# Performance work log

Hardware: AMD Instinct MI355X
Metric: run time of the kernel (lower is better)

Reference implementation:

```python
import jax, jax.numpy as jnp
import numpy as np
from jax import lax

SR = 7
HEADS = 8
EPS = 1e-5

def dwconv(x, w):
    # x: [B,C,H,W], w: [C,1,3,3] depthwise
    return lax.conv_general_dilated(x, w, (1, 1), 'SAME',
                                    feature_group_count=x.shape[1],
                                    dimension_numbers=('NCHW', 'OIHW', 'NCHW'))

def bn(x, g, b, m, v):
    # eval-mode BatchNorm2d over channel dim of [B,C,H,W]
    scale = g / jnp.sqrt(v + EPS)
    return x * scale[:, None, None] + (b - m * scale)[:, None, None]

def avgpool(x, k):
    B, C, H, W = x.shape
    return x.reshape(B, C, H // k, k, W // k, k).mean(axis=(3, 5))

def upsample(x, k):
    B, C, H, W = x.shape
    return jax.image.resize(x, (B, C, H * k, W * k), method='bilinear')


def setup_inputs() -> dict:
    key = jax.random.key(0)
    ks = jax.random.split(key, 12)
    B, N, C = 16, 3136, 256
    d = {}
    d['x'] = jax.random.normal(ks[0], (B, N, C), jnp.float32)
    d['Wv'] = jax.random.normal(ks[1], (C, C), jnp.float32) * 0.05
    d['conv1_w'] = jax.random.normal(ks[2], (C, 1, 3, 3), jnp.float32) * 0.05
    d['bn1_g'] = jnp.ones((C,), jnp.float32)
    d['bn1_b'] = jnp.zeros((C,), jnp.float32)
    d['bn1_m'] = jax.random.normal(ks[3], (C,), jnp.float32) * 0.05
    d['bn1_v'] = jax.random.uniform(ks[4], (C,), jnp.float32, 0.5, 1.5)
    d['conv2_w'] = jax.random.normal(ks[5], (C, 1, 3, 3), jnp.float32) * 0.05
    d['bn2_g'] = jnp.ones((C,), jnp.float32)
    d['bn2_b'] = jnp.zeros((C,), jnp.float32)
    d['bn2_m'] = jax.random.normal(ks[6], (C,), jnp.float32) * 0.05
    d['bn2_v'] = jax.random.uniform(ks[7], (C,), jnp.float32, 0.5, 1.5)
    d['vup_w'] = jax.random.normal(ks[8], (C, 1, 3, 3), jnp.float32) * 0.05
    d['bn3_g'] = jnp.ones((C,), jnp.float32)
    d['bn3_b'] = jnp.zeros((C,), jnp.float32)
    d['bn3_m'] = jax.random.normal(ks[9], (C,), jnp.float32) * 0.05
    d['bn3_v'] = jax.random.uniform(ks[10], (C,), jnp.float32, 0.5, 1.5)
    d['Wp'] = jax.random.normal(ks[11], (C, C), jnp.float32) * 0.05
    d['bp'] = jnp.zeros((C,), jnp.float32)
    return d


def reference(x, Wv, conv1_w, bn1_g, bn1_b, bn1_m, bn1_v,
              conv2_w, bn2_g, bn2_b, bn2_m, bn2_v,
              vup_w, bn3_g, bn3_b, bn3_m, bn3_v, Wp, bp):
    B, N, C = x.shape
    h = w = int(np.sqrt(N))
    hd = C // HEADS
    scale = C ** (-0.5)

    v = x @ Wv.T                                    # [B,N,C] (torch Linear, no bias)
    skip = v.reshape(B, h, w, C).transpose(0, 3, 1, 2)  # [B,C,h,w]

    s1 = bn(dwconv(skip, conv1_w), bn1_g, bn1_b, bn1_m, bn1_v)
    q = avgpool(s1, SR)                             # [B,C,h_,w_]
    s2 = bn(dwconv(jax.nn.gelu(s1, approximate=False), conv2_w),
            bn2_g, bn2_b, bn2_m, bn2_v)
    k = avgpool(s2, SR)                             # [B,C,h_,w_]
    skip_tok = jax.nn.gelu(s2, approximate=False).reshape(B, C, N).transpose(0, 2, 1)

    h_, w_ = h // SR, w // SR
    N_ = h_ * w_
    qh = q.reshape(B, HEADS, hd, N_).transpose(0, 1, 3, 2)   # [B,H,N_,d]
    kh = k.reshape(B, HEADS, hd, N_).transpose(0, 1, 3, 2)   # [B,H,N_,d]
    vh = v.reshape(B, N, HEADS, hd).transpose(0, 2, 1, 3)    # [B,H,N,d]

    attn = jnp.einsum('bhnd,bhmd->bhnm', qh, kh)             # [B,H,N_,N_]
    attn = attn.reshape(B * HEADS, N_, h_, w_)
    attn = upsample(attn, SR) * scale                        # [B*H,N_,h,w]
    attn = attn.reshape(B, HEADS, N_, N)
    attn = jax.nn.softmax(attn, axis=-1)

    o = jnp.einsum('bhnm,bhmd->bhnd', attn, vh)              # [B,H,N_,d]
    o = o.reshape(B, HEADS, h_, w_, hd).transpose(0, 1, 4, 2, 3).reshape(B, C, h_, w_)
    o = bn(dwconv(upsample(o, SR), vup_w), bn3_g, bn3_b, bn3_m, bn3_v)  # [B,C,h,w]

    out = o.reshape(B, C, N).transpose(0, 2, 1) + skip_tok
    out = out @ Wp.T + bp
    return out
```

## Files before the change

kernel.cpp:

```cpp
#include <hip/hip_runtime.h>
#include <math.h>

#define B_     16
#define H_IMG  56
#define W_IMG  56
#define N_TOK  3136
#define C_     256
#define C4_    64
#define NHEAD  8
#define HDIM   32
#define NCH    8

typedef float f32x4 __attribute__((ext_vector_type(4)));
typedef __bf16 bf16x8 __attribute__((ext_vector_type(8)));

__device__ __forceinline__ float geluf(float x) {
    return 0.5f * x * (1.0f + erff(x * 0.70710678118654752f));
}

__device__ __forceinline__ void up_coef(int o, int& i0, int& i1, float& t) {
    float f  = (float)(o - 3) * (1.0f / 7.0f);
    float fl = floorf(f);
    int   ii = (int)fl;
    t = f - fl;
    if (ii < 0)       { i0 = 0; i1 = 0; t = 0.0f; }
    else if (ii >= 7) { i0 = 7; i1 = 7; t = 0.0f; }
    else              { i0 = ii; i1 = ii + 1; }
}

__device__ __forceinline__ void split_bf16(float4 f, uint2& hi, uint2& lo) {
    unsigned u0 = __float_as_uint(f.x), u1 = __float_as_uint(f.y);
    unsigned u2 = __float_as_uint(f.z), u3 = __float_as_uint(f.w);
    unsigned h0 = u0 & 0xFFFF0000u, h1 = u1 & 0xFFFF0000u;
    unsigned h2 = u2 & 0xFFFF0000u, h3 = u3 & 0xFFFF0000u;
    hi = make_uint2((h0 >> 16) | h1, (h2 >> 16) | h3);
    float l0 = f.x - __uint_as_float(h0);
    float l1 = f.y - __uint_as_float(h1);
    float l2 = f.z - __uint_as_float(h2);
    float l3 = f.w - __uint_as_float(h3);
    lo = make_uint2((__float_as_uint(l0) >> 16) | (__float_as_uint(l1) & 0xFFFF0000u),
                    (__float_as_uint(l2) >> 16) | (__float_as_uint(l3) & 0xFFFF0000u));
}

__device__ __forceinline__ unsigned pack2_bf16(float a, float b) {
    __bf16 ha = (__bf16)a, hb = (__bf16)b;
    unsigned short ua = __builtin_bit_cast(unsigned short, ha);
    unsigned short ub = __builtin_bit_cast(unsigned short, hb);
    return (unsigned)ua | ((unsigned)ub << 16);
}

__device__ __forceinline__ void gload_lds16(const float* g, float* l) {
    __builtin_amdgcn_global_load_lds(
        (const __attribute__((address_space(1))) unsigned int*)g,
        (__attribute__((address_space(3))) unsigned int*)l, 16, 0, 0);
}

__global__ void prep_kernel(
    const float* __restrict__ w1, const float* __restrict__ w2, const float* __restrict__ w3,
    const float* __restrict__ g1, const float* __restrict__ b1, const float* __restrict__ m1, const float* __restrict__ v1,
    const float* __restrict__ g2, const float* __restrict__ b2, const float* __restrict__ m2, const float* __restrict__ v2,
    const float* __restrict__ g3, const float* __restrict__ b3, const float* __restrict__ m3, const float* __restrict__ v3,
    float* __restrict__ wT1, float* __restrict__ wT2, float* __restrict__ wT3,
    float* __restrict__ sc1, float* __restrict__ sh1,
    float* __restrict__ sc2, float* __restrict__ sh2,
    float* __restrict__ sc3, float* __restrict__ sh3)
{
    int c = threadIdx.x;
#pragma unroll
    for (int t = 0; t < 9; ++t) {
        wT1[t * C_ + c] = w1[c * 9 + t];
        wT2[t * C_ + c] = w2[c * 9 + t];
        wT3[t * C_ + c] = w3[c * 9 + t];
    }
    float s1 = g1[c] * rsqrtf(v1[c] + 1e-5f); sc1[c] = s1; sh1[c] = b1[c] - m1[c] * s1;
    float s2 = g2[c] * rsqrtf(v2[c] + 1e-5f); sc2[c] = s2; sh2[c] = b2[c] - m2[c] * s2;
    float s3 = g3[c] * rsqrtf(v3[c] + 1e-5f); sc3[c] = s3; sh3[c] = b3[c] - m3[c] * s3;
}

__global__ __launch_bounds__(256, 2) void gemm_nt_mfma_kernel(
    const float* __restrict__ A,
    const float* __restrict__ Bm,
    const float* __restrict__ bias,
    float* __restrict__ C,
    int M, int N)
{
    __shared__ float lds[8192];
    const int tid  = threadIdx.x;
    const int nb   = N >> 7;
    const int bx   = blockIdx.x % nb;
    const int by   = blockIdx.x / nb;
    const int lane = tid & 63;
    const int wv   = tid >> 6;
    const int wr   = wv >> 1, wc = wv & 1;
    const int l15  = lane & 15, kb = lane >> 4;

    const float* Abase = A  + (size_t)(by * 128) * 256;
    const float* Bbase = Bm + (size_t)(bx * 128) * 256;

    f32x4 acc[4][4];
#pragma unroll
    for (int m = 0; m < 4; ++m)
#pragma unroll
        for (int n = 0; n < 4; ++n) acc[m][n] = (f32x4)(0.0f);

    int srow[4], ssk[4];
#pragma unroll
    for (int i = 0; i < 4; ++i) {
        int u = i * 256 + tid;
        srow[i] = u >> 3;
        ssk[i]  = ((u & 7) ^ (srow[i] & 7)) << 2;
    }

#pragma unroll
    for (int k0 = 0; k0 < 256; k0 += 32) {
        __syncthreads();
#pragma unroll
        for (int i = 0; i < 4; ++i) {
            int u = i * 256 + tid;
            gload_lds16(Abase + (size_t)srow[i] * 256 + k0 + ssk[i], &lds[u * 4]);
        }
#pragma unroll
        for (int i = 0; i < 4; ++i) {
            int u = i * 256 + tid;
            gload_lds16(Bbase + (size_t)srow[i] * 256 + k0 + ssk[i], &lds[4096 + u * 4]);
        }
        __syncthreads();

        bf16x8 ah[4], al[4], bh[4], bl[4];
#pragma unroll
        for (int m = 0; m < 4; ++m) {
            int r = wr * 64 + m * 16 + l15;
            float4 f0 = *(const float4*)&lds[r * 32 + ((((kb * 2)    ) ^ (r & 7)) << 2)];
            float4 f1 = *(const float4*)&lds[r * 32 + ((((kb * 2) + 1) ^ (r & 7)) << 2)];
            uint2 h0, l0, h1, l1;
            split_bf16(f0, h0, l0);
            split_bf16(f1, h1, l1);
            ah[m] = __builtin_bit_cast(bf16x8, make_uint4(h0.x, h0.y, h1.x, h1.y));
            al[m] = __builtin_bit_cast(bf16x8, make_uint4(l0.x, l0.y, l1.x, l1.y));
        }
#pragma unroll
        for (int n = 0; n < 4; ++n) {
            int r = wc * 64 + n * 16 + l15;
            float4 f0 = *(const float4*)&lds[4096 + r * 32 + ((((kb * 2)    ) ^ (r & 7)) << 2)];
            float4 f1 = *(const float4*)&lds[4096 + r * 32 + ((((kb * 2) + 1) ^ (r & 7)) << 2)];
            uint2 h0, l0, h1, l1;
            split_bf16(f0, h0, l0);
            split_bf16(f1, h1, l1);
            bh[n] = __builtin_bit_cast(bf16x8, make_uint4(h0.x, h0.y, h1.x, h1.y));
            bl[n] = __builtin_bit_cast(bf16x8, make_uint4(l0.x, l0.y, l1.x, l1.y));
        }
#pragma unroll
        for (int m = 0; m < 4; ++m)
#pragma unroll
            for (int n = 0; n < 4; ++n) {
                acc[m][n] = __builtin_amdgcn_mfma_f32_16x16x32_bf16(ah[m], bh[n], acc[m][n], 0, 0, 0);
                acc[m][n] = __builtin_amdgcn_mfma_f32_16x16x32_bf16(ah[m], bl[n], acc[m][n], 0, 0, 0);
                acc[m][n] = __builtin_amdgcn_mfma_f32_16x16x32_bf16(al[m], bh[n], acc[m][n], 0, 0, 0);
            }
    }

    const int rb = by * 128 + wr * 64 + kb * 4;
    const int cb = bx * 128 + wc * 64 + l15;
#pragma unroll
    for (int n = 0; n < 4; ++n) {
        int col = cb + n * 16;
        float bv = bias ? bias[col] : 0.0f;
#pragma unroll
        for (int m = 0; m < 4; ++m) {
            int row = rb + m * 16;
#pragma unroll
            for (int r = 0; r < 4; ++r)
                C[(size_t)(row + r) * N + col] = acc[m][n][r] + bv;
        }
    }
}

__global__ __launch_bounds__(256, 4) void dwconv_bn_pool_gelu_kernel(
    const float* __restrict__ in, const float* __restrict__ wT,
    const float* __restrict__ scv, const float* __restrict__ shv,
    float* __restrict__ outg, float* __restrict__ pool)
{
    const int blk = blockIdx.x;
    const int xcd = blk & 7;
    const int j   = blk >> 3;
    const int b   = xcd + 8 * (j >> 6);
    const int g   = j & 63;
    const int gy  = g >> 3, gx = g & 7;
    const int tid = threadIdx.x;
    const int c4  = tid & 63;
    const int wv  = tid >> 6;
    const int c0  = c4 * 4;

    float4 wr[9];
#pragma unroll
    for (int t = 0; t < 9; ++t) wr[t] = *(const float4*)(wT + t * C_ + c0);
    const float4 sc = *(const float4*)(scv + c0);
    const float4 sh = *(const float4*)(shv + c0);

    const int x0 = gx * 7, y0 = gy * 7;
    const float* inb = in + (size_t)b * N_TOK * C_;
    float4 acc = make_float4(0, 0, 0, 0);

    for (int p = wv; p < 49; p += 4) {
        int py = p / 7, px = p - py * 7;
        int y = y0 + py, x = x0 + px;
        float cx = 0.f, cy = 0.f, cz = 0.f, cw = 0.f;
#pragma unroll
        for (int dy = -1; dy <= 1; ++dy) {
            int yy = y + dy;
            if (yy < 0 || yy >= H_IMG) continue;
#pragma unroll
            for (int dx = -1; dx <= 1; ++dx) {
                int xx = x + dx;
                if (xx < 0 || xx >= W_IMG) continue;
                const float4 iv = *(const float4*)(inb + (size_t)(yy * W_IMG + xx) * C_ + c0);
                const float4 w  = wr[(dy + 1) * 3 + (dx + 1)];
                cx = fmaf(iv.x, w.x, cx);
                cy = fmaf(iv.y, w.y, cy);
                cz = fmaf(iv.z, w.z, cz);
                cw = fmaf(iv.w, w.w, cw);
            }
        }
        float vx = cx * sc.x + sh.x;
        float vy = cy * sc.y + sh.y;
        float vz = cz * sc.z + sh.z;
        float vw = cw * sc.w + sh.w;
        acc.x += vx; acc.y += vy; acc.z += vz; acc.w += vw;
        *(float4*)(outg + ((size_t)b * N_TOK + y * W_IMG + x) * C_ + c0) =
            make_float4(geluf(vx), geluf(vy), geluf(vz), geluf(vw));
    }

    __shared__ float4 ps[4][64];
    ps[wv][c4] = acc;
    __syncthreads();
    if (tid < 64) {
        float4 s  = ps[0][tid];
        float4 t1 = ps[1][tid];
        float4 t2 = ps[2][tid];
        float4 t3 = ps[3][tid];
        const float r = 1.0f / 49.0f;
        *(float4*)(pool + ((size_t)b * 64 + g) * C_ + tid * 4) = make_float4(
            (s.x + t1.x + t2.x + t3.x) * r, (s.y + t1.y + t2.y + t3.y) * r,
            (s.z + t1.z + t2.z + t3.z) * r, (s.w + t1.w + t2.w + t3.w) * r);
    }
}

__global__ __launch_bounds__(256, 3) void dwconv_up_bn_add_kernel(
    const float* __restrict__ osm,
    const float* __restrict__ wT,
    const float* __restrict__ scv, const float* __restrict__ shv,
    const float* __restrict__ add_,
    float* __restrict__ out)
{
    const int blk = blockIdx.x;
    const int xcd = blk & 7;
    const int j   = blk >> 3;
    const int b   = xcd + 8 * (j >> 6);
    const int g   = j & 63;
    const int gy  = g >> 3, gx = g & 7;
    const int tid = threadIdx.x;
    const int c4  = tid & 63;
    const int wv  = tid >> 6;
    const int c0  = c4 * 4;

    float4 wr[9];
#pragma unroll
    for (int t = 0; t < 9; ++t) wr[t] = *(const float4*)(wT + t * C_ + c0);
    const float4 sc = *(const float4*)(scv + c0);
    const float4 sh = *(const float4*)(shv + c0);

    const float* ob = osm + (size_t)b * 64 * C_ + c0;
    const int cry0 = max(gy - 1, 0), cry1 = gy, cry2 = min(gy + 1, 7);
    const int crx0 = max(gx - 1, 0), crx1 = gx, crx2 = min(gx + 1, 7);

    for (int cpass = 0; cpass < 2; ++cpass) {
        const int xi = wv + cpass * 4;
        if (xi >= 7) break;
        const int x = gx * 7 + xi;

        float xt[3]; int rixv[3]; bool xval[3];
#pragma unroll
        for (int e = 0; e < 3; ++e) {
            int xx = x - 1 + e;
            xval[e] = (xx >= 0 && xx < W_IMG);
            if (xval[e]) {
                int i0, i1; float t;
                up_coef(xx, i0, i1, t);
                rixv[e] = i0 - gx + 1;
                xt[e]   = t;
            } else { rixv[e] = 0; xt[e] = 0.f; }
        }

        float4 CX[3][3];
#pragma unroll
        for (int ri = 0; ri < 3; ++ri) {
            const int rowc = (ri == 0) ? cry0 : ((ri == 1) ? cry1 : cry2);
            const float4 p0 = *(const float4*)(ob + (size_t)(rowc * 8 + crx0) * C_);
            const float4 p1 = *(const float4*)(ob + (size_t)(rowc * 8 + crx1) * C_);
            const float4 p2 = *(const float4*)(ob + (size_t)(rowc * 8 + crx2) * C_);
#pragma unroll
            for (int e = 0; e < 3; ++e) {
                const bool h2 = rixv[e] != 0;
                float lox = h2 ? p1.x : p0.x, hix = h2 ? p2.x : p1.x;
                float loy = h2 ? p1.y : p0.y, hiy = h2 ? p2.y : p1.y;
                float loz = h2 ? p1.z : p0.z, hiz = h2 ? p2.z : p1.z;
                float low = h2 ? p1.w : p0.w, hiw = h2 ? p2.w : p1.w;
                const float t = xt[e];
                float vx = fmaf(t, hix - lox, lox);
                float vy = fmaf(t, hiy - loy, loy);
                float vz = fmaf(t, hiz - loz, loz);
                float vw = fmaf(t, hiw - low, low);
                if (!xval[e]) { vx = vy = vz = vw = 0.f; }
                CX[ri][e] = make_float4(vx, vy, vz, vw);
            }
        }

#define UPROW(YY, U)                                                          \
        {                                                                     \
            int i0_, i1_; float t_;                                           \
            up_coef((YY), i0_, i1_, t_);                                      \
            const bool h2_ = (i0_ - gy + 1) != 0;                             \
            _Pragma("unroll")                                                 \
            for (int e = 0; e < 3; ++e) {                                     \
                const float4 lo = h2_ ? CX[1][e] : CX[0][e];                  \
                const float4 hi = h2_ ? CX[2][e] : CX[1][e];                  \
                U[e] = make_float4(fmaf(t_, hi.x - lo.x, lo.x),               \
                                   fmaf(t_, hi.y - lo.y, lo.y),               \
                                   fmaf(t_, hi.z - lo.z, lo.z),               \
                                   fmaf(t_, hi.w - lo.w, lo.w));              \
            }                                                                 \
        }

        float4 Um[3], U0[3], Up[3];
        UPROW(gy * 7 - 1, Um);
        UPROW(gy * 7,     U0);
#pragma unroll
        for (int y7 = 0; y7 < 7; ++y7) {
            const int y = gy * 7 + y7;
            UPROW(y + 1, Up);
            float ax = 0.f, ay = 0.f, az = 0.f, aw = 0.f;
            if (!(gy == 0 && y7 == 0)) {
#pragma unroll
                for (int e = 0; e < 3; ++e) {
                    const float4 w = wr[e];
                    ax = fmaf(Um[e].x, w.x, ax); ay = fmaf(Um[e].y, w.y, ay);
                    az = fmaf(Um[e].z, w.z, az); aw = fmaf(Um[e].w, w.w, aw);
                }
            }
#pragma unroll
            for (int e = 0; e < 3; ++e) {
                const float4 w = wr[3 + e];
                ax = fmaf(U0[e].x, w.x, ax); ay = fmaf(U0[e].y, w.y, ay);
                az = fmaf(U0[e].z, w.z, az); aw = fmaf(U0[e].w, w.w, aw);
            }
            if (!(gy == 7 && y7 == 6)) {
#pragma unroll
                for (int e = 0; e < 3; ++e) {
                    const float4 w = wr[6 + e];
                    ax = fmaf(Up[e].x, w.x, ax); ay = fmaf(Up[e].y, w.y, ay);
                    az = fmaf(Up[e].z, w.z, az); aw = fmaf(Up[e].w, w.w, aw);
                }
            }
            const size_t pix = (size_t)b * N_TOK + (size_t)y * W_IMG + x;
            const float4 av = *(const float4*)(add_ + pix * C_ + c0);
            *(float4*)(out + pix * C_ + c0) = make_float4(
                ax * sc.x + sh.x + av.x, ay * sc.y + sh.y + av.y,
                az * sc.z + sh.z + av.z, aw * sc.w + sh.w + av.w);
#pragma unroll
            for (int e = 0; e < 3; ++e) { Um[e] = U0[e]; U0[e] = Up[e]; }
        }
#undef UPROW
    }
}

__global__ __launch_bounds__(256) void qk_kernel(
    const float* __restrict__ q, const float* __restrict__ k,
    float* __restrict__ attnL, float* __restrict__ mrow_g)
{
    int bh = blockIdx.x;
    int b = bh >> 3, head = bh & 7;
    __shared__ float qs[64][33];
    __shared__ float ks[64][33];
    int tid = threadIdx.x;
    for (int t = tid; t < 512; t += 256) {
        int i = t >> 3, dq = (t & 7) * 4;
        const float4 qv = *(const float4*)(q + ((size_t)(b * 64 + i) * C_ + head * 32 + dq));
        const float4 kv = *(const float4*)(k + ((size_t)(b * 64 + i) * C_ + head * 32 + dq));
        qs[i][dq + 0] = qv.x; qs[i][dq + 1] = qv.y; qs[i][dq + 2] = qv.z; qs[i][dq + 3] = qv.w;
        ks[i][dq + 0] = kv.x; ks[i][dq + 1] = kv.y; ks[i][dq + 2] = kv.z; ks[i][dq + 3] = kv.w;
    }
    __syncthreads();
    int i  = tid >> 2;
    int jb = (tid & 3) * 16;
    float qr[32];
#pragma unroll
    for (int d = 0; d < 32; ++d) qr[d] = qs[i][d];
    float* outp = attnL + (size_t)bh * 4096 + i * 64 + jb;
    float mloc = -1e30f;
#pragma unroll
    for (int j = 0; j < 16; ++j) {
        float s = 0.f;
#pragma unroll
        for (int d = 0; d < 32; ++d) s = fmaf(qr[d], ks[jb + j][d], s);
        float sv = s * 0.0625f;
        outp[j] = sv;
        mloc = fmaxf(mloc, sv);
    }
    mloc = fmaxf(mloc, __shfl_xor(mloc, 1));
    mloc = fmaxf(mloc, __shfl_xor(mloc, 2));
    if ((tid & 3) == 0) mrow_g[bh * 64 + i] = mloc;
}

#define S_ALS 0
#define S_P   1792
#define S_VH  4096
#define S_VL  5248
#define S_RY  6400
#define S_ZP  7168
__global__ __launch_bounds__(256, 4) void attn_pv_kernel(
    const float* __restrict__ attnL,
    const float* __restrict__ mrow_g,
    const float* __restrict__ v,
    float* __restrict__ part_o,
    float* __restrict__ part_z)
{
    __shared__ unsigned sm[7424];
    float* smf = (float*)sm;

    const int blk   = blockIdx.x;
    const int xcd   = blk & 7;
    const int r8    = blk >> 3;
    const int b     = xcd + 8 * (r8 >> 6);
    const int rem   = r8 & 63;
    const int head  = rem >> 3;
    const int chunk = rem & 7;
    const int bh    = b * 8 + head;
    const int jb    = min(max(chunk - 1, 0), 5);

    const int tid  = threadIdx.x;
    const int lane = tid & 63;
    const int w    = tid >> 6;
    const int l15  = lane & 15, kb = lane >> 4;
    const int i    = tid >> 2;
    const int dg   = tid & 3;

    for (int u = tid; u < 384; u += 256) {
        int row = u / 6, cc = u % 6;
        float4 va = *(const float4*)(attnL + (size_t)bh * 4096 + row * 64 + jb * 8 + cc * 4);
        *(float4*)&smf[S_ALS + row * 28 + cc * 4] = va;
    }
    sm[S_P + (tid >> 2) * 36 + 28 + (tid & 3)] = 0;
    {
        int base = (tid < 128) ? S_VH : S_VL;
        int q2 = tid & 127;
        sm[base + (q2 >> 2) * 36 + 28 + (q2 & 3)] = 0;
    }
    const float mr = mrow_g[bh * 64 + i];

    int   x0a[14]; float txa[14];
#pragma unroll
    for (int j = 0; j < 14; ++j) {
        int i0, i1; float t;
        up_coef(dg * 14 + j, i0, i1, t);
        x0a[j] = i0; txa[j] = t;
    }

    f32x4 acc[2];
    acc[0] = (f32x4)(0.0f); acc[1] = (f32x4)(0.0f);
    float zacc = 0.0f;

    for (int rr = 0; rr < 7; ++rr) {
        const int y = chunk * 7 + rr;
        __syncthreads();

        float4 va, vb;
        if (tid < 224) {
            int x2 = tid >> 3, d0 = (tid & 7) * 4;
            const float* vp = v + ((size_t)b * N_TOK + y * W_IMG + 2 * x2) * C_ + head * 32 + d0;
            va = *(const float4*)vp;
            vb = *(const float4*)(vp + C_);
        }
        {
            int y0, y1; float ty;
            up_coef(y, y0, y1, ty);
#pragma unroll
            for (int kk2 = dg; kk2 < 9; kk2 += 4) {
                int ks2 = kk2 < 8 ? kk2 : 7;
                float a0 = smf[S_ALS + i * 28 + (y0 - jb) * 8 + ks2];
                float a1 = smf[S_ALS + i * 28 + (y1 - jb) * 8 + ks2];
                smf[S_RY + i * 12 + kk2] = fmaf(ty, a1 - a0, a0) - mr;
            }
        }
        if (tid < 224) {
            int x2 = tid >> 3, d0 = (tid & 7) * 4;
            float ae[4] = {va.x, va.y, va.z, va.w};
            float be[4] = {vb.x, vb.y, vb.z, vb.w};
#pragma unroll
            for (int j = 0; j < 4; ++j) {
                unsigned ua = __float_as_uint(ae[j]), ha = ua & 0xFFFF0000u;
                unsigned ub = __float_as_uint(be[j]), hb2 = ub & 0xFFFF0000u;
                sm[S_VH + (d0 + j) * 36 + x2] = (ha >> 16) | hb2;
                float la = ae[j] - __uint_as_float(ha);
                float lb = be[j] - __uint_as_float(hb2);
                sm[S_VL + (d0 + j) * 36 + x2] =
                    (__float_as_uint(la) >> 16) | (__float_as_uint(lb) & 0xFFFF0000u);
            }
        }
        __syncthreads();

#pragma unroll
        for (int j = 0; j < 7; ++j) {
            float r0 = smf[S_RY + i * 12 + x0a[2 * j]];
            float r1 = smf[S_RY + i * 12 + x0a[2 * j] + 1];
            float l0 = fmaf(txa[2 * j], r1 - r0, r0);
            float r2 = smf[S_RY + i * 12 + x0a[2 * j + 1]];
            float r3 = smf[S_RY + i * 12 + x0a[2 * j + 1] + 1];
            float l1 = fmaf(txa[2 * j + 1], r3 - r2, r2);
            float p0 = __expf(l0), p1 = __expf(l1);
            zacc += p0 + p1;
            sm[S_P + i * 36 + dg * 7 + j] = pack2_bf16(p0, p1);
        }
        __syncthreads();

#pragma unroll
        for (int s = 0; s < 2; ++s) {
            bf16x8 pa = *(const bf16x8*)&sm[S_P + (w * 16 + l15) * 36 + s * 16 + kb * 4];
#pragma unroll
            for (int n = 0; n < 2; ++n) {
                bf16x8 bhv = *(const bf16x8*)&sm[S_VH + (n * 16 + l15) * 36 + s * 16 + kb * 4];
                bf16x8 blv = *(const bf16x8*)&sm[S_VL + (n * 16 + l15) * 36 + s * 16 + kb * 4];
                acc[n] = __builtin_amdgcn_mfma_f32_16x16x32_bf16(pa, bhv, acc[n], 0, 0, 0);
                acc[n] = __builtin_amdgcn_mfma_f32_16x16x32_bf16(pa, blv, acc[n], 0, 0, 0);
            }
        }
    }

    smf[S_ZP + i * 4 + dg] = zacc;
    __syncthreads();
    if (tid < 64) {
        float zt = smf[S_ZP + tid * 4] + smf[S_ZP + tid * 4 + 1] +
                   smf[S_ZP + tid * 4 + 2] + smf[S_ZP + tid * 4 + 3];
        part_z[((size_t)bh * NCH + chunk) * 64 + tid] = zt;
    }
    const int row4 = (lane >> 4) * 4;
#pragma unroll
    for (int n = 0; n < 2; ++n)
#pragma unroll
        for (int r2 = 0; r2 < 4; ++r2) {
            int i2 = w * 16 + row4 + r2;
            int d  = n * 16 + l15;
            part_o[(((size_t)bh * NCH + chunk) * 64 + i2) * 32 + d] = acc[n][r2];
        }
}

__global__ __launch_bounds__(256) void combine_kernel(
    const float* __restrict__ part_o, const float* __restrict__ part_z,
    float* __restrict__ o_small)
{
    int idx = blockIdx.x * 256 + threadIdx.x;
    if (idx >= B_ * 64 * C_) return;
    int c = idx % C_;
    int g = (idx / C_) % 64;
    int b = idx / (C_ * 64);
    int head = c >> 5, d = c & 31;
    int bh = b * 8 + head;
    float oo = 0.f, zz = 0.f;
    for (int ch = 0; ch < NCH; ++ch) {
        oo += part_o[(((size_t)bh * NCH + ch) * 64 + g) * 32 + d];
        zz += part_z[((size_t)bh * NCH + ch) * 64 + g];
    }
    o_small[idx] = oo / zz;
}

extern "C" void kernel_launch(void* const* d_in, const int* in_sizes, int n_in,
                              void* d_out, int out_size, void* d_ws, size_t ws_size,
                              hipStream_t stream)
{
    const float* x    = (const float*)d_in[0];
    const float* Wv   = (const float*)d_in[1];
    const float* c1w  = (const float*)d_in[2];
    const float* b1g  = (const float*)d_in[3];
    const float* b1b  = (const float*)d_in[4];
    const float* b1m  = (const float*)d_in[5];
    const float* b1v  = (const float*)d_in[6];
    const float* c2w  = (const float*)d_in[7];
    const float* b2g  = (const float*)d_in[8];
    const float* b2b  = (const float*)d_in[9];
    const float* b2m  = (const float*)d_in[10];
    const float* b2v  = (const float*)d_in[11];
    const float* vupw = (const float*)d_in[12];
    const float* b3g  = (const float*)d_in[13];
    const float* b3b  = (const float*)d_in[14];
    const float* b3m  = (const float*)d_in[15];
    const float* b3v  = (const float*)d_in[16];
    const float* Wp   = (const float*)d_in[17];
    const float* bp   = (const float*)d_in[18];
    float* out = (float*)d_out;
    float* ws  = (float*)d_ws;

    const size_t SZ = (size_t)B_ * N_TOK * C_;
    float* v       = ws;
    float* s1g     = v   + SZ;
    float* s2g     = s1g + SZ;
    float* q       = s2g + SZ;
    float* kk      = q  + (size_t)B_ * 64 * C_;
    float* attnL   = kk + (size_t)B_ * 64 * C_;
    float* part_o  = attnL  + (size_t)B_ * 8 * 64 * 64;
    float* part_z  = part_o + (size_t)B_ * 8 * NCH * 64 * 32;
    float* o_small = part_z + (size_t)B_ * 8 * NCH * 64;
    float* wT1     = o_small + (size_t)B_ * 64 * C_;
    float* wT2     = wT1 + 9 * C_;
    float* wT3     = wT2 + 9 * C_;
    float* sc1     = wT3 + 9 * C_;
    float* sh1     = sc1 + C_;
    float* sc2     = sh1 + C_;
    float* sh2     = sc2 + C_;
    float* sc3     = sh2 + C_;
    float* sh3     = sc3 + C_;
    float* mrow_g  = sh3 + C_;

    const int M = B_ * N_TOK;

    prep_kernel<<<1, 256, 0, stream>>>(c1w, c2w, vupw,
        b1g, b1b, b1m, b1v, b2g, b2b, b2m, b2v, b3g, b3b, b3m, b3v,
        wT1, wT2, wT3, sc1, sh1, sc2, sh2, sc3, sh3);
    gemm_nt_mfma_kernel<<<(M / 128) * (C_ / 128), 256, 0, stream>>>(x, Wv, nullptr, v, M, C_);
    dwconv_bn_pool_gelu_kernel<<<1024, 256, 0, stream>>>(v, wT1, sc1, sh1, s1g, q);
    dwconv_bn_pool_gelu_kernel<<<1024, 256, 0, stream>>>(s1g, wT2, sc2, sh2, s2g, kk);
    qk_kernel<<<B_ * 8, 256, 0, stream>>>(q, kk, attnL, mrow_g);
    attn_pv_kernel<<<B_ * 8 * NCH, 256, 0, stream>>>(attnL, mrow_g, v, part_o, part_z);
    combine_kernel<<<B_ * 64 * C_ / 256, 256, 0, stream>>>(part_o, part_z, o_small);
    dwconv_up_bn_add_kernel<<<1024, 256, 0, stream>>>(o_small, wT3, sc3, sh3, s2g, v);
    gemm_nt_mfma_kernel<<<(M / 128) * (C_ / 128), 256, 0, stream>>>(v, Wp, bp, out, M, C_);
}
```

Baseline: 217.2 us.

## Double-buffer LDS tiles in the MFMA projection GEMM

Doubles the GEMM's shared-memory tile buffer and issues the global-to-LDS loads for the next K slice before computing on the current one. This overlaps global memory latency with the split-bf16 MFMA work and drops one barrier per K iteration. In exchange, LDS use per block doubles to 64KB, which can limit how many blocks share a CU. Only the projection GEMMs change; the conv and attention kernels are untouched.

```diff
diff --git a/kernel.cpp b/kernel.cpp
--- a/kernel.cpp
+++ b/kernel.cpp
@@ -84,7 +84,7 @@
     float* __restrict__ C,
     int M, int N)
 {
-    __shared__ float lds[8192];
+    __shared__ float lds[16384];
     const int tid  = threadIdx.x;
     const int nb   = N >> 7;
     const int bx   = blockIdx.x % nb;
@@ -111,27 +111,39 @@
         ssk[i]  = ((u & 7) ^ (srow[i] & 7)) << 2;
     }
 
+#define STAGE(base, k0)                                                        \
+    {                                                                          \
+        _Pragma("unroll")                                                      \
+        for (int i_ = 0; i_ < 4; ++i_) {                                       \
+            int u_ = i_ * 256 + tid;                                           \
+            gload_lds16(Abase + (size_t)srow[i_] * 256 + (k0) + ssk[i_],       \
+                        &lds[(base) + u_ * 4]);                                \
+        }                                                                      \
+        _Pragma("unroll")                                                      \
+        for (int i_ = 0; i_ < 4; ++i_) {                                       \
+            int u_ = i_ * 256 + tid;                                           \
+            gload_lds16(Bbase + (size_t)srow[i_] * 256 + (k0) + ssk[i_],       \
+                        &lds[(base) + 4096 + u_ * 4]);                         \
+        }                                                                      \
+    }
+
+    STAGE(0, 0);
+
 #pragma unroll
     for (int k0 = 0; k0 < 256; k0 += 32) {
+        const int cur = (k0 >> 5) & 1;
+        const int cb_ = cur * 8192;
         __syncthreads();
-#pragma unroll
-        for (int i = 0; i < 4; ++i) {
-            int u = i * 256 + tid;
-            gload_lds16(Abase + (size_t)srow[i] * 256 + k0 + ssk[i], &lds[u * 4]);
-        }
-#pragma unroll
-        for (int i = 0; i < 4; ++i) {
-            int u = i * 256 + tid;
-            gload_lds16(Bbase + (size_t)srow[i] * 256 + k0 + ssk[i], &lds[4096 + u * 4]);
-        }
-        __syncthreads();
+        if (k0 + 32 < 256) {
+            STAGE((cur ^ 1) * 8192, k0 + 32);
+        }
 
         bf16x8 ah[4], al[4], bh[4], bl[4];
 #pragma unroll
         for (int m = 0; m < 4; ++m) {
             int r = wr * 64 + m * 16 + l15;
-            float4 f0 = *(const float4*)&lds[r * 32 + ((((kb * 2)    ) ^ (r & 7)) << 2)];
-            float4 f1 = *(const float4*)&lds[r * 32 + ((((kb * 2) + 1) ^ (r & 7)) << 2)];
+            float4 f0 = *(const float4*)&lds[cb_ + r * 32 + ((((kb * 2)    ) ^ (r & 7)) << 2)];
+            float4 f1 = *(const float4*)&lds[cb_ + r * 32 + ((((kb * 2) + 1) ^ (r & 7)) << 2)];
             uint2 h0, l0, h1, l1;
             split_bf16(f0, h0, l0);
             split_bf16(f1, h1, l1);
@@ -141,8 +153,8 @@
 #pragma unroll
         for (int n = 0; n < 4; ++n) {
             int r = wc * 64 + n * 16 + l15;
-            float4 f0 = *(const float4*)&lds[4096 + r * 32 + ((((kb * 2)    ) ^ (r & 7)) << 2)];
-            float4 f1 = *(const float4*)&lds[4096 + r * 32 + ((((kb * 2) + 1) ^ (r & 7)) << 2)];
+            float4 f0 = *(const float4*)&lds[cb_ + 4096 + r * 32 + ((((kb * 2)    ) ^ (r & 7)) << 2)];
+            float4 f1 = *(const float4*)&lds[cb_ + 4096 + r * 32 + ((((kb * 2) + 1) ^ (r & 7)) << 2)];
             uint2 h0, l0, h1, l1;
             split_bf16(f0, h0, l0);
             split_bf16(f1, h1, l1);
@@ -158,6 +170,7 @@
                 acc[m][n] = __builtin_amdgcn_mfma_f32_16x16x32_bf16(al[m], bh[n], acc[m][n], 0, 0, 0);
             }
     }
+#undef STAGE
 
     const int rb = by * 128 + wr * 64 + kb * 4;
     const int cb = bx * 128 + wc * 64 + l15;
```

Result: slower. 224.6 us (+3.4%).

## Fold conv weights into upsample coefficients and swizzle GEMM blocks across XCDs

Applied to the files above, without the earlier changes.

The upsample+depthwise-conv kernel now hoists the 3x3 coarse-patch loads out of the column-pass loop. It also folds the horizontal interpolation weights into the conv taps, so each output row needs only three vertical lerps of precomputed per-column sums instead of building and shifting interpolated row buffers. Separately, the MFMA GEMM remaps block IDs so consecutive tiles land on the same XCD, aiming for better L2 reuse. The arithmetic restructuring changes floating-point summation order and adds a few more registers.

```diff
diff --git a/kernel.cpp b/kernel.cpp
--- a/kernel.cpp
+++ b/kernel.cpp
@@ -87,8 +87,12 @@
     __shared__ float lds[8192];
     const int tid  = threadIdx.x;
     const int nb   = N >> 7;
-    const int bx   = blockIdx.x % nb;
-    const int by   = blockIdx.x / nb;
+    const int nwg  = (M >> 7) * nb;
+    const int cpx  = nwg >> 3;
+    const int bid  = blockIdx.x;
+    const int swz  = (bid & 7) * cpx + (bid >> 3);
+    const int bx   = swz % nb;
+    const int by   = swz / nb;
     const int lane = tid & 63;
     const int wv   = tid >> 6;
     const int wr   = wv >> 1, wc = wv & 1;
@@ -270,106 +274,86 @@
     const float4 sh = *(const float4*)(shv + c0);
 
     const float* ob = osm + (size_t)b * 64 * C_ + c0;
-    const int cry0 = max(gy - 1, 0), cry1 = gy, cry2 = min(gy + 1, 7);
-    const int crx0 = max(gx - 1, 0), crx1 = gx, crx2 = min(gx + 1, 7);
+    const int cry0 = max(gy - 1, 0), cry2 = min(gy + 1, 7);
+    const int crx0 = max(gx - 1, 0), crx2 = min(gx + 1, 7);
+    float4 P[3][3];
+#pragma unroll
+    for (int ri = 0; ri < 3; ++ri) {
+        const int rowc = (ri == 0) ? cry0 : ((ri == 1) ? gy : cry2);
+        P[ri][0] = *(const float4*)(ob + (size_t)(rowc * 8 + crx0) * C_);
+        P[ri][1] = *(const float4*)(ob + (size_t)(rowc * 8 + gx)   * C_);
+        P[ri][2] = *(const float4*)(ob + (size_t)(rowc * 8 + crx2) * C_);
+    }
 
     for (int cpass = 0; cpass < 2; ++cpass) {
         const int xi = wv + cpass * 4;
         if (xi >= 7) break;
         const int x = gx * 7 + xi;
 
-        float xt[3]; int rixv[3]; bool xval[3];
+        float axw[3][3];
 #pragma unroll
         for (int e = 0; e < 3; ++e) {
             int xx = x - 1 + e;
-            xval[e] = (xx >= 0 && xx < W_IMG);
-            if (xval[e]) {
+            if (xx >= 0 && xx < W_IMG) {
                 int i0, i1; float t;
                 up_coef(xx, i0, i1, t);
-                rixv[e] = i0 - gx + 1;
-                xt[e]   = t;
-            } else { rixv[e] = 0; xt[e] = 0.f; }
-        }
-
-        float4 CX[3][3];
-#pragma unroll
-        for (int ri = 0; ri < 3; ++ri) {
-            const int rowc = (ri == 0) ? cry0 : ((ri == 1) ? cry1 : cry2);
-            const float4 p0 = *(const float4*)(ob + (size_t)(rowc * 8 + crx0) * C_);
-            const float4 p1 = *(const float4*)(ob + (size_t)(rowc * 8 + crx1) * C_);
-            const float4 p2 = *(const float4*)(ob + (size_t)(rowc * 8 + crx2) * C_);
-#pragma unroll
-            for (int e = 0; e < 3; ++e) {
-                const bool h2 = rixv[e] != 0;
-                float lox = h2 ? p1.x : p0.x, hix = h2 ? p2.x : p1.x;
-                float loy = h2 ? p1.y : p0.y, hiy = h2 ? p2.y : p1.y;
-                float loz = h2 ? p1.z : p0.z, hiz = h2 ? p2.z : p1.z;
-                float low = h2 ? p1.w : p0.w, hiw = h2 ? p2.w : p1.w;
-                const float t = xt[e];
-                float vx = fmaf(t, hix - lox, lox);
-                float vy = fmaf(t, hiy - loy, loy);
-                float vz = fmaf(t, hiz - loz, loz);
-                float vw = fmaf(t, hiw - low, low);
-                if (!xval[e]) { vx = vy = vz = vw = 0.f; }
-                CX[ri][e] = make_float4(vx, vy, vz, vw);
-            }
-        }
-
-#define UPROW(YY, U)                                                          \
-        {                                                                     \
-            int i0_, i1_; float t_;                                           \
-            up_coef((YY), i0_, i1_, t_);                                      \
-            const bool h2_ = (i0_ - gy + 1) != 0;                             \
-            _Pragma("unroll")                                                 \
-            for (int e = 0; e < 3; ++e) {                                     \
-                const float4 lo = h2_ ? CX[1][e] : CX[0][e];                  \
-                const float4 hi = h2_ ? CX[2][e] : CX[1][e];                  \
-                U[e] = make_float4(fmaf(t_, hi.x - lo.x, lo.x),               \
-                                   fmaf(t_, hi.y - lo.y, lo.y),               \
-                                   fmaf(t_, hi.z - lo.z, lo.z),               \
-                                   fmaf(t_, hi.w - lo.w, lo.w));              \
-            }                                                                 \
-        }
-
-        float4 Um[3], U0[3], Up[3];
-        UPROW(gy * 7 - 1, Um);
-        UPROW(gy * 7,     U0);
+                const bool r0 = (i0 - gx + 1) == 0;
+                axw[e][0] = r0 ? (1.0f - t) : 0.0f;
+                axw[e][1] = r0 ? t : (1.0f - t);
+                axw[e][2] = r0 ? 0.0f : t;
+            } else {
+                axw[e][0] = 0.0f; axw[e][1] = 0.0f; axw[e][2] = 0.0f;
+            }
+        }
+
+        float4 S[3][3];
+#pragma unroll
+        for (int d = 0; d < 3; ++d) {
+            float4 cw0, cw1, cw2;
+#pragma unroll
+            for (int ci = 0; ci < 3; ++ci) {
+                float4 c;
+                c.x = wr[d*3+0].x * axw[0][ci] + wr[d*3+1].x * axw[1][ci] + wr[d*3+2].x * axw[2][ci];
+                c.y = wr[d*3+0].y * axw[0][ci] + wr[d*3+1].y * axw[1][ci] + wr[d*3+2].y * axw[2][ci];
+                c.z = wr[d*3+0].z * axw[0][ci] + wr[d*3+1].z * axw[1][ci] + wr[d*3+2].z * axw[2][ci];
+                c.w = wr[d*3+0].w * axw[0][ci] + wr[d*3+1].w * axw[1][ci] + wr[d*3+2].w * axw[2][ci];
+                if (ci == 0) cw0 = c; else if (ci == 1) cw1 = c; else cw2 = c;
+            }
+#pragma unroll
+            for (int ri = 0; ri < 3; ++ri) {
+                float4 s;
+                s.x = cw0.x * P[ri][0].x + cw1.x * P[ri][1].x + cw2.x * P[ri][2].x;
+                s.y = cw0.y * P[ri][0].y + cw1.y * P[ri][1].y + cw2.y * P[ri][2].y;
+                s.z = cw0.z * P[ri][0].z + cw1.z * P[ri][1].z + cw2.z * P[ri][2].z;
+                s.w = cw0.w * P[ri][0].w + cw1.w * P[ri][1].w + cw2.w * P[ri][2].w;
+                S[d][ri] = s;
+            }
+        }
+
 #pragma unroll
         for (int y7 = 0; y7 < 7; ++y7) {
             const int y = gy * 7 + y7;
-            UPROW(y + 1, Up);
             float ax = 0.f, ay = 0.f, az = 0.f, aw = 0.f;
-            if (!(gy == 0 && y7 == 0)) {
-#pragma unroll
-                for (int e = 0; e < 3; ++e) {
-                    const float4 w = wr[e];
-                    ax = fmaf(Um[e].x, w.x, ax); ay = fmaf(Um[e].y, w.y, ay);
-                    az = fmaf(Um[e].z, w.z, az); aw = fmaf(Um[e].w, w.w, aw);
-                }
-            }
-#pragma unroll
-            for (int e = 0; e < 3; ++e) {
-                const float4 w = wr[3 + e];
-                ax = fmaf(U0[e].x, w.x, ax); ay = fmaf(U0[e].y, w.y, ay);
-                az = fmaf(U0[e].z, w.z, az); aw = fmaf(U0[e].w, w.w, aw);
-            }
-            if (!(gy == 7 && y7 == 6)) {
-#pragma unroll
-                for (int e = 0; e < 3; ++e) {
-                    const float4 w = wr[6 + e];
-                    ax = fmaf(Up[e].x, w.x, ax); ay = fmaf(Up[e].y, w.y, ay);
-                    az = fmaf(Up[e].z, w.z, az); aw = fmaf(Up[e].w, w.w, aw);
-                }
+#pragma unroll
+            for (int d = 0; d < 3; ++d) {
+                const int yy = y + d - 1;
+                if (yy < 0 || yy >= H_IMG) continue;
+                int i0, i1; float ty;
+                up_coef(yy, i0, i1, ty);
+                const bool hi2 = (i0 - gy + 1) != 0;
+                const float4 lo = hi2 ? S[d][1] : S[d][0];
+                const float4 hi = hi2 ? S[d][2] : S[d][1];
+                ax += fmaf(ty, hi.x - lo.x, lo.x);
+                ay += fmaf(ty, hi.y - lo.y, lo.y);
+                az += fmaf(ty, hi.z - lo.z, lo.z);
+                aw += fmaf(ty, hi.w - lo.w, lo.w);
             }
             const size_t pix = (size_t)b * N_TOK + (size_t)y * W_IMG + x;
             const float4 av = *(const float4*)(add_ + pix * C_ + c0);
             *(float4*)(out + pix * C_ + c0) = make_float4(
                 ax * sc.x + sh.x + av.x, ay * sc.y + sh.y + av.y,
                 az * sc.z + sh.z + av.z, aw * sc.w + sh.w + av.w);
-#pragma unroll
-            for (int e = 0; e < 3; ++e) { Um[e] = U0[e]; U0[e] = Up[e]; }
-        }
-#undef UPROW
+        }
     }
 }
 
```

New measurement: 211.3 us. -2.7%, faster.
